# Performance work log

Measured on AMD Instinct MI355X. Metric: run time of the kernel, lower is better.

Reference implementation:

```python
import jax, jax.numpy as jnp
import numpy as np

N_MEL = 80
ENC_POS = 512 + 32  # encoder_output_dim + positional_embedding_dim
RNN = 1024
PRE = 256
B = 32
T = 800


def setup_inputs() -> dict:
    key = jax.random.key(0)
    ks = jax.random.split(key, 20)
    s = 0.05
    inp = {
        'duration_outputs': jax.random.normal(ks[0], (B, T, ENC_POS), jnp.float32),
        'decoder_inputs': jax.random.normal(ks[1], (B, N_MEL, T), jnp.float32),
        'memory_lengths': jax.random.randint(ks[2], (B,), 1, 200),
        # Prenet (no bias)
        'W1': jax.random.normal(ks[3], (PRE, N_MEL), jnp.float32) * s,
        'W2': jax.random.normal(ks[4], (PRE, PRE), jnp.float32) * s,
        # LSTMCellNorm 1: input = PRE + ENC_POS
        'Wih1': jax.random.normal(ks[5], (4 * RNN, PRE + ENC_POS), jnp.float32) * s,
        'Whh1': jax.random.normal(ks[6], (4 * RNN, RNN), jnp.float32) * s,
        'b1': jnp.zeros((4 * RNN,), jnp.float32),
        'g1': jnp.ones((4 * RNN,), jnp.float32),
        'be1': jnp.zeros((4 * RNN,), jnp.float32),
        # LSTMCellNorm 2
        'Wih2': jax.random.normal(ks[7], (4 * RNN, RNN), jnp.float32) * s,
        'Whh2': jax.random.normal(ks[8], (4 * RNN, RNN), jnp.float32) * s,
        'b2': jnp.zeros((4 * RNN,), jnp.float32),
        'g2': jnp.ones((4 * RNN,), jnp.float32),
        'be2': jnp.zeros((4 * RNN,), jnp.float32),
        # Linear projection: RNN + ENC_POS -> N_MEL
        'Wp': jax.random.normal(ks[9], (N_MEL, RNN + ENC_POS), jnp.float32) * s,
        'bp': jnp.zeros((N_MEL,), jnp.float32),
        # Dropout masks (prenet p=0.5 always on; decoder p=0.1 in training)
        'pm1': jax.random.bernoulli(ks[10], 0.5, (T + 1, B, PRE)).astype(jnp.float32) / 0.5,
        'pm2': jax.random.bernoulli(ks[11], 0.5, (T + 1, B, PRE)).astype(jnp.float32) / 0.5,
        'dm1': jax.random.bernoulli(ks[12], 0.9, (T, B, RNN)).astype(jnp.float32) / 0.9,
        'dm2': jax.random.bernoulli(ks[13], 0.9, (T, B, RNN)).astype(jnp.float32) / 0.9,
    }
    return inp


def _ln(z, g, b):
    m = jnp.mean(z, -1, keepdims=True)
    v = jnp.var(z, -1, keepdims=True)
    return (z - m) * jax.lax.rsqrt(v + 1e-5) * g + b


def _cell(x, h, c, Wih, Whh, bias, g, be):
    # layer-normalized LSTM cell: LN over the 4H pre-activation gates
    gates = _ln(x @ Wih.T + h @ Whh.T + bias, g, be)
    i, f, gg, o = jnp.split(gates, 4, axis=-1)
    c = jax.nn.sigmoid(f) * c + jax.nn.sigmoid(i) * jnp.tanh(gg)
    h = jax.nn.sigmoid(o) * jnp.tanh(c)
    return h, c


def reference(duration_outputs, decoder_inputs, memory_lengths,
              W1, W2, Wih1, Whh1, b1, g1, be1, Wih2, Whh2, b2, g2, be2,
              Wp, bp, pm1, pm2, dm1, dm2):
    Bv = duration_outputs.shape[0]
    H = Whh1.shape[1]
    # parse_decoder_inputs: [B, n_mel, T] -> [T, B, n_mel] (n_frames_per_step=1)
    dec = jnp.transpose(decoder_inputs, (2, 0, 1))
    Tv = dec.shape[0]
    go = jnp.zeros((1, Bv, dec.shape[2]), dec.dtype)
    dec = jnp.concatenate([go, dec], axis=0)  # [T+1, B, n_mel]
    # Prenet (dropout always active)
    x = jax.nn.relu(dec @ W1.T) * pm1
    x = jax.nn.relu(x @ W2.T) * pm2  # [T+1, B, PRE]
    dur = jnp.transpose(duration_outputs, (1, 0, 2))  # [T, B, 544]

    def step(carry, xs):
        h1, c1, h2, c2 = carry
        pre_t, dur_t, m1, m2 = xs
        h1, c1 = _cell(jnp.concatenate([pre_t, dur_t], -1), h1, c1, Wih1, Whh1, b1, g1, be1)
        h1 = h1 * m1  # dropped hidden is also carried, matching torch
        h2, c2 = _cell(h1, h2, c2, Wih2, Whh2, b2, g2, be2)
        h2 = h2 * m2
        out = jnp.concatenate([h2, dur_t], -1) @ Wp.T + bp
        return (h1, c1, h2, c2), out

    z = jnp.zeros((Bv, H), duration_outputs.dtype)
    _, outs = jax.lax.scan(step, (z, z, z, z), (x[:Tv], dur[:Tv], dm1, dm2))
    mel = jnp.transpose(outs, (1, 0, 2))  # [B, T, n_mel]
    mel = mel.reshape(Bv, -1, N_MEL)
    return jnp.transpose(mel, (0, 2, 1))  # [B, n_mel, T]
```

## Files before the change

### kernel.cpp

```cpp
#include <hip/hip_runtime.h>

#define TT 800
#define BB 32
#define HH 1024
#define G4 4096
#define PRE 256
#define DUR 544
#define XK 800
#define KA 1824
#define KB 2048
#define NM 80
#define KP 1568

#define SA 1864
#define SB 2056
#define SA1 104

#define OFF_WIH1B  0ull
#define OFF_WHH1B  6553600ull
#define OFF_WIH2B  14942208ull
#define OFF_WHH2B  23330816ull
#define OFF_WPB    31719424ull
#define OFF_W1B    31970304ull
#define OFF_W2B    32019456ull
#define OFF_XCAT   32150528ull
#define OFF_X1     73110528ull
#define OFF_H1H    86217728ull
#define OFF_H2H    138646528ull
#define OFF_PART1  191075328ull
#define OFF_PART2  191337472ull
#define OFF_FLAGS  191599616ull
#define FLAG_BYTES 217600ull
#define WS_NEEDED  (OFF_FLAGS + FLAG_BYTES)

#define LDS_SLAB_OFF  131584
#define LDS_STAT_OFF  148480
#define LDS_RED_OFF   148736
#define LDS_HPK_OFF   149760
#define LDS_TOTAL     150272

typedef __attribute__((ext_vector_type(8))) _Float16 f16x8;
typedef __attribute__((ext_vector_type(4))) float f32x4;
typedef unsigned long long ull;

__device__ __forceinline__ unsigned short f2h(float f) {
    _Float16 h = (_Float16)f;
    return __builtin_bit_cast(unsigned short, h);
}
__device__ __forceinline__ float sigf(float x) { return 1.f / (1.f + __expf(-x)); }
__device__ __forceinline__ float tanh_fast(float x) { return 1.f - 2.f / (__expf(2.f * x) + 1.f); }

__device__ __forceinline__ f16x8 ldg8(const unsigned short* p) {
    return *reinterpret_cast<const f16x8*>(p);
}

__device__ __forceinline__ f16x8 ld_h16(const ull* p) {
    union { ull u[2]; f16x8 v; } x;
    x.u[0] = __hip_atomic_load(p,     __ATOMIC_RELAXED, __HIP_MEMORY_SCOPE_AGENT);
    x.u[1] = __hip_atomic_load(p + 1, __ATOMIC_RELAXED, __HIP_MEMORY_SCOPE_AGENT);
    return x.v;
}
__device__ __forceinline__ float ld_cf(const float* p) {
    return __hip_atomic_load(p, __ATOMIC_RELAXED, __HIP_MEMORY_SCOPE_AGENT);
}
__device__ __forceinline__ void st_cf(float* p, float v) {
    __hip_atomic_store(p, v, __ATOMIC_RELAXED, __HIP_MEMORY_SCOPE_AGENT);
}

__device__ __forceinline__ void spin_until(int* p, int target) {
    while (__hip_atomic_load(p, __ATOMIC_RELAXED, __HIP_MEMORY_SCOPE_AGENT) < target)
        __builtin_amdgcn_s_sleep(1);
}

#define WAIT_VM0() __builtin_amdgcn_s_waitcnt(0x0F70)

__global__ void cvt_kernel(const float* __restrict__ src, unsigned short* __restrict__ dst, int n) {
    for (int i = blockIdx.x * blockDim.x + threadIdx.x; i < n; i += gridDim.x * blockDim.x)
        dst[i] = f2h(src[i]);
}

__global__ void cvt_w1_kernel(const float* __restrict__ w1, unsigned short* __restrict__ dst) {
    int i = blockIdx.x * blockDim.x + threadIdx.x;
    if (i >= 256 * 96) return;
    int j = i / 96, m = i % 96;
    dst[i] = (m < 80) ? f2h(w1[j * 80 + m]) : 0;
}

__global__ void pack_dur_kernel(const float* __restrict__ dur, unsigned short* __restrict__ xcat) {
    int n = TT * BB * DUR;
    for (int i = blockIdx.x * blockDim.x + threadIdx.x; i < n; i += gridDim.x * blockDim.x) {
        int t = i / (BB * DUR);
        int r = i % (BB * DUR);
        int b = r / DUR, e = r % DUR;
        xcat[(size_t)(t * BB + b) * XK + PRE + e] = f2h(dur[(size_t)b * (TT * DUR) + t * DUR + e]);
    }
}

__global__ __launch_bounds__(256) void prenet1_kernel(const float* __restrict__ din,
                                                      const unsigned short* __restrict__ w1b,
                                                      const float* __restrict__ pm1,
                                                      unsigned short* __restrict__ x1b) {
    int t = blockIdx.x;
    __shared__ unsigned short decs[32 * SA1];
    int tid = threadIdx.x;
    for (int idx = tid; idx < 32 * 96; idx += 256) {
        int b = idx / 96, m = idx % 96;
        float v = (m < 80 && t > 0) ? din[(size_t)b * 64000 + m * 800 + (t - 1)] : 0.f;
        decs[b * SA1 + m] = f2h(v);
    }
    __syncthreads();
    int lane = tid & 63, wid = tid >> 6;
    int l15 = lane & 15, quad = lane >> 4;
    int kblk = quad * 8;
    #pragma unroll
    for (int i = 0; i < 8; i++) {
        int tt = wid * 8 + i;
        int Mt = tt & 1, Nt = tt >> 1;
        f32x4 acc = {0.f, 0.f, 0.f, 0.f};
        int arow = (Mt * 16 + l15) * SA1 + kblk;
        int brow = (Nt * 16 + l15) * 96 + kblk;
        #pragma unroll
        for (int kk = 0; kk < 3; kk++) {
            f16x8 a = *reinterpret_cast<const f16x8*>(&decs[arow + kk * 32]);
            f16x8 b = ldg8(w1b + brow + kk * 32);
            acc = __builtin_amdgcn_mfma_f32_16x16x32_f16(a, b, acc, 0, 0, 0);
        }
        int n = Nt * 16 + l15;
        #pragma unroll
        for (int r = 0; r < 4; r++) {
            int b_row = Mt * 16 + quad * 4 + r;
            float v = fmaxf(acc[r], 0.f) * pm1[(size_t)(t * BB + b_row) * PRE + n];
            x1b[(size_t)(t * BB + b_row) * PRE + n] = f2h(v);
        }
    }
}

__global__ __launch_bounds__(256) void prenet2_kernel(const unsigned short* __restrict__ x1b,
                                                      const unsigned short* __restrict__ w2b,
                                                      const float* __restrict__ pm2,
                                                      unsigned short* __restrict__ xcat) {
    int t = blockIdx.x;
    int tid = threadIdx.x;
    int lane = tid & 63, wid = tid >> 6;
    int l15 = lane & 15, quad = lane >> 4;
    int kblk = quad * 8;
    #pragma unroll
    for (int i = 0; i < 8; i++) {
        int tt = wid * 8 + i;
        int Mt = tt & 1, Nt = tt >> 1;
        f32x4 acc = {0.f, 0.f, 0.f, 0.f};
        const unsigned short* arow = x1b + (size_t)(t * BB + Mt * 16 + l15) * PRE + kblk;
        const unsigned short* brow = w2b + (size_t)(Nt * 16 + l15) * PRE + kblk;
        #pragma unroll
        for (int kk = 0; kk < 8; kk++) {
            f16x8 a = ldg8(arow + kk * 32);
            f16x8 b = ldg8(brow + kk * 32);
            acc = __builtin_amdgcn_mfma_f32_16x16x32_f16(a, b, acc, 0, 0, 0);
        }
        int n = Nt * 16 + l15;
        #pragma unroll
        for (int r = 0; r < 4; r++) {
            int b_row = Mt * 16 + quad * 4 + r;
            float v = fmaxf(acc[r], 0.f) * pm2[(size_t)(t * BB + b_row) * PRE + n];
            xcat[(size_t)(t * BB + b_row) * XK + n] = f2h(v);
        }
    }
}

__global__ __launch_bounds__(256, 1) void persistent_kernel(
    const unsigned short* __restrict__ xcat,
    const unsigned short* __restrict__ wih1b, const unsigned short* __restrict__ whh1b,
    const unsigned short* __restrict__ wih2b, const unsigned short* __restrict__ whh2b,
    const float* __restrict__ b1, const float* __restrict__ g1, const float* __restrict__ be1,
    const float* __restrict__ b2, const float* __restrict__ g2, const float* __restrict__ be2,
    const float* __restrict__ dm1, const float* __restrict__ dm2,
    unsigned short* __restrict__ h1h, unsigned short* __restrict__ h2h,
    float* __restrict__ part1, float* __restrict__ part2,
    int* __restrict__ flags) {

    extern __shared__ char smem[];
    unsigned short* W = (unsigned short*)smem;
    float* slab = (float*)(smem + LDS_SLAB_OFF);
    float* stat = (float*)(smem + LDS_STAT_OFF);
    float* red  = (float*)(smem + LDS_RED_OFF);
    unsigned short* hpack = (unsigned short*)(smem + LDS_HPK_OFF);

    int wg = blockIdx.x;
    bool isA = wg < 128;
    int w = isA ? wg : wg - 128;
    int tid = threadIdx.x;
    int lane = tid & 63;
    int kid = tid >> 6;
    int l15 = lane & 15, quad = lane >> 4;
    int koff = quad * 8;

    int* r_h1     = flags + 800;
    int* gbase    = flags + 3200;
    int* r_stats  = isA ? flags : (flags + 1600);
    int* r_hmy    = isA ? (flags + 800) : (flags + 2400);
    int* g_stats  = isA ? gbase : (gbase + 25600);
    int* g_hmy    = isA ? (gbase + 12800) : (gbase + 38400);
    float* part   = isA ? part1 : part2;
    float* statg  = part + 4 * 8192;
    int gidx = w >> 3;
    bool isRed = (w == 0);

    if (isA) {
        for (int idx = tid; idx < 32 * KA; idx += 256) {
            int r = idx / KA, k = idx % KA;
            int grow = (r >> 3) * HH + w * 8 + (r & 7);
            W[r * SA + k] = (k < XK) ? wih1b[(size_t)grow * XK + k]
                                     : whh1b[(size_t)grow * HH + (k - XK)];
        }
    } else {
        for (int idx = tid; idx < 32 * KB; idx += 256) {
            int r = idx / KB, k = idx % KB;
            int grow = (r >> 3) * HH + w * 8 + (r & 7);
            W[r * SB + k] = (k < HH) ? wih2b[(size_t)grow * HH + k]
                                     : whh2b[(size_t)grow * HH + (k - HH)];
        }
    }

    int n_s = tid & 31, ms = (tid >> 5) * 4;
    int gate_ns = (n_s >> 3) * HH + w * 8 + (n_s & 7);
    float bsum = isA ? b1[gate_ns] : b2[gate_ns];

    int pb = tid & 31, pu = tid >> 5;
    int unit = w * 8 + pu;
    float g1v[4], bev[4];
    {
        const float* gs = isA ? g1 : g2;
        const float* bs = isA ? be1 : be2;
        #pragma unroll
        for (int g = 0; g < 4; g++) { g1v[g] = gs[g * HH + unit]; bev[g] = bs[g * HH + unit]; }
    }
    const float* dms = isA ? dm1 : dm2;
    unsigned short* hout = isA ? h1h : h2h;
    float* myslab = slab + kid * (32 * 33);
    int stride_slab = 33;
    float creg = 0.f;
    __syncthreads();

    for (int t = 0; t < TT; t++) {
        int slot = t & 3;
        f32x4 a00 = {0,0,0,0}, a01 = {0,0,0,0}, a10 = {0,0,0,0}, a11 = {0,0,0,0};

        if (isA) {
            const unsigned short* xb = xcat + (size_t)(t * BB) * XK;
            for (int kk = kid; kk < 25; kk += 4) {
                int k0 = kk * 32 + koff;
                f16x8 x0 = ldg8(xb + (size_t)(l15)      * XK + k0);
                f16x8 x1 = ldg8(xb + (size_t)(16 + l15) * XK + k0);
                f16x8 w0 = *(const f16x8*)&W[(l15)      * SA + k0];
                f16x8 w1 = *(const f16x8*)&W[(16 + l15) * SA + k0];
                a00 = __builtin_amdgcn_mfma_f32_16x16x32_f16(x0, w0, a00, 0, 0, 0);
                a01 = __builtin_amdgcn_mfma_f32_16x16x32_f16(x0, w1, a01, 0, 0, 0);
                a10 = __builtin_amdgcn_mfma_f32_16x16x32_f16(x1, w0, a10, 0, 0, 0);
                a11 = __builtin_amdgcn_mfma_f32_16x16x32_f16(x1, w1, a11, 0, 0, 0);
            }
            if (t > 0) {
                if (tid == 0) spin_until(&r_hmy[t - 1], 16);
                __syncthreads();
                const unsigned short* hb = h1h + (size_t)((t - 1) * BB) * HH;
                for (int kk = kid; kk < 32; kk += 4) {
                    int k0 = kk * 32 + koff;
                    f16x8 x0 = ld_h16((const ull*)(hb + (size_t)(l15)      * HH + k0));
                    f16x8 x1 = ld_h16((const ull*)(hb + (size_t)(16 + l15) * HH + k0));
                    f16x8 w0 = *(const f16x8*)&W[(l15)      * SA + XK + k0];
                    f16x8 w1 = *(const f16x8*)&W[(16 + l15) * SA + XK + k0];
                    a00 = __builtin_amdgcn_mfma_f32_16x16x32_f16(x0, w0, a00, 0, 0, 0);
                    a01 = __builtin_amdgcn_mfma_f32_16x16x32_f16(x0, w1, a01, 0, 0, 0);
                    a10 = __builtin_amdgcn_mfma_f32_16x16x32_f16(x1, w0, a10, 0, 0, 0);
                    a11 = __builtin_amdgcn_mfma_f32_16x16x32_f16(x1, w1, a11, 0, 0, 0);
                }
            }
        } else {
            if (t > 0) {
                if (tid == 0) spin_until(&r_hmy[t - 1], 16);
                __syncthreads();
                const unsigned short* hb = h2h + (size_t)((t - 1) * BB) * HH;
                for (int kk = kid; kk < 32; kk += 4) {
                    int k0 = kk * 32 + koff;
                    f16x8 x0 = ld_h16((const ull*)(hb + (size_t)(l15)      * HH + k0));
                    f16x8 x1 = ld_h16((const ull*)(hb + (size_t)(16 + l15) * HH + k0));
                    f16x8 w0 = *(const f16x8*)&W[(l15)      * SB + HH + k0];
                    f16x8 w1 = *(const f16x8*)&W[(16 + l15) * SB + HH + k0];
                    a00 = __builtin_amdgcn_mfma_f32_16x16x32_f16(x0, w0, a00, 0, 0, 0);
                    a01 = __builtin_amdgcn_mfma_f32_16x16x32_f16(x0, w1, a01, 0, 0, 0);
                    a10 = __builtin_amdgcn_mfma_f32_16x16x32_f16(x1, w0, a10, 0, 0, 0);
                    a11 = __builtin_amdgcn_mfma_f32_16x16x32_f16(x1, w1, a11, 0, 0, 0);
                }
            }
            if (tid == 0) spin_until(&r_h1[t], 16);
            __syncthreads();
            const unsigned short* hb = h1h + (size_t)(t * BB) * HH;
            for (int kk = kid; kk < 32; kk += 4) {
                int k0 = kk * 32 + koff;
                f16x8 x0 = ld_h16((const ull*)(hb + (size_t)(l15)      * HH + k0));
                f16x8 x1 = ld_h16((const ull*)(hb + (size_t)(16 + l15) * HH + k0));
                f16x8 w0 = *(const f16x8*)&W[(l15)      * SB + k0];
                f16x8 w1 = *(const f16x8*)&W[(16 + l15) * SB + k0];
                a00 = __builtin_amdgcn_mfma_f32_16x16x32_f16(x0, w0, a00, 0, 0, 0);
                a01 = __builtin_amdgcn_mfma_f32_16x16x32_f16(x0, w1, a01, 0, 0, 0);
                a10 = __builtin_amdgcn_mfma_f32_16x16x32_f16(x1, w0, a10, 0, 0, 0);
                a11 = __builtin_amdgcn_mfma_f32_16x16x32_f16(x1, w1, a11, 0, 0, 0);
            }
        }

        #pragma unroll
        for (int r = 0; r < 4; r++) {
            int m0 = quad * 4 + r;
            myslab[(l15)      * stride_slab + m0]      = a00[r];
            myslab[(16 + l15) * stride_slab + m0]      = a01[r];
            myslab[(l15)      * stride_slab + 16 + m0] = a10[r];
            myslab[(16 + l15) * stride_slab + 16 + m0] = a11[r];
        }
        __syncthreads();

        {
            int base = n_s * stride_slab + ms;
            #pragma unroll
            for (int j = 0; j < 4; j++) {
                float v = slab[base + j] + slab[1056 + base + j]
                        + slab[2112 + base + j] + slab[3168 + base + j] + bsum;
                slab[base + j] = v;
            }
        }
        __syncthreads();

        if (tid < 64) {
            int b = tid & 31, st = tid >> 5;
            float s = 0.f;
            #pragma unroll 8
            for (int n = 0; n < 32; n++) { float v = slab[n * stride_slab + b]; s += st ? v * v : v; }
            st_cf(&part[slot * 8192 + w * 64 + tid], s);
        }
        if (tid == 0) {
            WAIT_VM0();
            int old = __hip_atomic_fetch_add(&g_stats[t * 16 + gidx], 1,
                                             __ATOMIC_RELAXED, __HIP_MEMORY_SCOPE_AGENT);
            if (old == 7)
                __hip_atomic_fetch_add(&r_stats[t], 1,
                                       __ATOMIC_RELAXED, __HIP_MEMORY_SCOPE_AGENT);
        }

        if (isRed) {
            if (tid == 0) spin_until(&r_stats[t], 16);
            __syncthreads();
            {
                const float* pp = part + slot * 8192;
                float s = 0.f;
                int wp = tid >> 6, j = tid & 63;
                #pragma unroll
                for (int i = 0; i < 32; i++)
                    s += ld_cf(&pp[(wp + i * 4) * 64 + j]);
                red[tid] = s;
            }
            __syncthreads();
            if (tid < 64)
                st_cf(&statg[slot * 64 + tid],
                      red[tid] + red[64 + tid] + red[128 + tid] + red[192 + tid]);
            if (tid == 0) {
                WAIT_VM0();
                __hip_atomic_fetch_add(&r_stats[t], 1,
                                       __ATOMIC_RELAXED, __HIP_MEMORY_SCOPE_AGENT);
            }
        }

        if (tid == 0) spin_until(&r_stats[t], 17);
        __syncthreads();
        if (tid < 64) stat[tid] = ld_cf(&statg[slot * 64 + tid]);
        __syncthreads();

        {
            float mean = stat[pb] * (1.f / 4096.f);
            float var = stat[32 + pb] * (1.f / 4096.f) - mean * mean;
            float rs = rsqrtf(var + 1e-5f);
            float z[4];
            #pragma unroll
            for (int g = 0; g < 4; g++)
                z[g] = (slab[(g * 8 + pu) * stride_slab + pb] - mean) * rs * g1v[g] + bev[g];
            float iv = sigf(z[0]), fv = sigf(z[1]), gv = tanh_fast(z[2]), ov = sigf(z[3]);
            creg = fv * creg + iv * gv;
            float h = ov * tanh_fast(creg);
            h *= dms[(size_t)(t * BB + pb) * HH + unit];
            hpack[pb * 8 + pu] = f2h(h);
        }
        __syncthreads();

        if (tid < 64) {
            int b = tid >> 1, half = tid & 1;
            ull v = *(const ull*)((const char*)hpack + tid * 8);
            __hip_atomic_store((ull*)(hout + (size_t)(t * BB + b) * HH + w * 8 + half * 4),
                               v, __ATOMIC_RELAXED, __HIP_MEMORY_SCOPE_AGENT);
        }
        if (tid == 0) {
            WAIT_VM0();
            int old = __hip_atomic_fetch_add(&g_hmy[t * 16 + gidx], 1,
                                             __ATOMIC_RELAXED, __HIP_MEMORY_SCOPE_AGENT);
            if (old == 7)
                __hip_atomic_fetch_add(&r_hmy[t], 1,
                                       __ATOMIC_RELAXED, __HIP_MEMORY_SCOPE_AGENT);
        }
    }
}

__global__ __launch_bounds__(256) void projection_kernel(const unsigned short* __restrict__ h2h,
                                                         const unsigned short* __restrict__ xcat,
                                                         const unsigned short* __restrict__ wpb,
                                                         const float* __restrict__ bp,
                                                         float* __restrict__ out) {
    int t = blockIdx.x;
    int tid = threadIdx.x;
    int lane = tid & 63, wid = tid >> 6;
    int l15 = lane & 15, quad = lane >> 4;
    int kblk = quad * 8;
    #pragma unroll
    for (int i = 0; i < 3; i++) {
        int tt = wid + i * 4;
        if (tt >= 10) break;
        int Mt = tt & 1, Nt = tt >> 1;
        f32x4 acc = {0.f, 0.f, 0.f, 0.f};
        int b_row = Mt * 16 + l15;
        const unsigned short* h2row = h2h + (size_t)(t * BB + b_row) * HH + kblk;
        const unsigned short* brow = wpb + (size_t)(Nt * 16 + l15) * KP + kblk;
        #pragma unroll
        for (int kk = 0; kk < 32; kk++) {
            f16x8 a = ldg8(h2row + kk * 32);
            f16x8 b = ldg8(brow + kk * 32);
            acc = __builtin_amdgcn_mfma_f32_16x16x32_f16(a, b, acc, 0, 0, 0);
        }
        const unsigned short* drow = xcat + (size_t)(t * BB + b_row) * XK + PRE + kblk;
        #pragma unroll
        for (int kk = 0; kk < 17; kk++) {
            f16x8 a = ldg8(drow + kk * 32);
            f16x8 b = ldg8(brow + HH + kk * 32);
            acc = __builtin_amdgcn_mfma_f32_16x16x32_f16(a, b, acc, 0, 0, 0);
        }
        int mel = Nt * 16 + l15;
        float bpv = bp[mel];
        #pragma unroll
        for (int r = 0; r < 4; r++) {
            int b = Mt * 16 + quad * 4 + r;
            out[(size_t)b * 64000 + mel * 800 + t] = acc[r] + bpv;
        }
    }
}

extern "C" void kernel_launch(void* const* d_in, const int* in_sizes, int n_in,
                              void* d_out, int out_size, void* d_ws, size_t ws_size,
                              hipStream_t stream) {
    (void)in_sizes; (void)n_in; (void)out_size;
    const float* dur  = (const float*)d_in[0];
    const float* din  = (const float*)d_in[1];
    const float* W1   = (const float*)d_in[3];
    const float* W2   = (const float*)d_in[4];
    const float* Wih1 = (const float*)d_in[5];
    const float* Whh1 = (const float*)d_in[6];
    const float* b1   = (const float*)d_in[7];
    const float* g1   = (const float*)d_in[8];
    const float* be1  = (const float*)d_in[9];
    const float* Wih2 = (const float*)d_in[10];
    const float* Whh2 = (const float*)d_in[11];
    const float* b2   = (const float*)d_in[12];
    const float* g2   = (const float*)d_in[13];
    const float* be2  = (const float*)d_in[14];
    const float* Wp   = (const float*)d_in[15];
    const float* bp   = (const float*)d_in[16];
    const float* pm1  = (const float*)d_in[17];
    const float* pm2  = (const float*)d_in[18];
    const float* dm1  = (const float*)d_in[19];
    const float* dm2  = (const float*)d_in[20];
    float* out = (float*)d_out;
    char* ws = (char*)d_ws;
    if (ws_size < WS_NEEDED) return;

    unsigned short* wih1b = (unsigned short*)(ws + OFF_WIH1B);
    unsigned short* whh1b = (unsigned short*)(ws + OFF_WHH1B);
    unsigned short* wih2b = (unsigned short*)(ws + OFF_WIH2B);
    unsigned short* whh2b = (unsigned short*)(ws + OFF_WHH2B);
    unsigned short* wpb   = (unsigned short*)(ws + OFF_WPB);
    unsigned short* w1b   = (unsigned short*)(ws + OFF_W1B);
    unsigned short* w2b   = (unsigned short*)(ws + OFF_W2B);
    unsigned short* xcat  = (unsigned short*)(ws + OFF_XCAT);
    unsigned short* x1b   = (unsigned short*)(ws + OFF_X1);
    unsigned short* h1h   = (unsigned short*)(ws + OFF_H1H);
    unsigned short* h2h   = (unsigned short*)(ws + OFF_H2H);
    float* part1 = (float*)(ws + OFF_PART1);
    float* part2 = (float*)(ws + OFF_PART2);
    int* flags   = (int*)(ws + OFF_FLAGS);

    hipMemsetAsync(flags, 0, FLAG_BYTES, stream);

    int thr = 256;
    cvt_kernel<<<4096, thr, 0, stream>>>(Wih1, wih1b, G4 * XK);
    cvt_kernel<<<4096, thr, 0, stream>>>(Whh1, whh1b, G4 * HH);
    cvt_kernel<<<4096, thr, 0, stream>>>(Wih2, wih2b, G4 * HH);
    cvt_kernel<<<4096, thr, 0, stream>>>(Whh2, whh2b, G4 * HH);
    cvt_kernel<<<512,  thr, 0, stream>>>(Wp, wpb, NM * KP);
    cvt_w1_kernel<<<(256 * 96 + 255) / 256, thr, 0, stream>>>(W1, w1b);
    cvt_kernel<<<256,  thr, 0, stream>>>(W2, w2b, 256 * 256);

    prenet1_kernel<<<TT, thr, 0, stream>>>(din, w1b, pm1, x1b);
    prenet2_kernel<<<TT, thr, 0, stream>>>(x1b, w2b, pm2, xcat);
    pack_dur_kernel<<<8192, thr, 0, stream>>>(dur, xcat);

    hipFuncSetAttribute((const void*)persistent_kernel,
                        hipFuncAttributeMaxDynamicSharedMemorySize, LDS_TOTAL);
    persistent_kernel<<<256, thr, LDS_TOTAL, stream>>>(
        xcat, wih1b, whh1b, wih2b, whh2b,
        b1, g1, be1, b2, g2, be2, dm1, dm2,
        h1h, h2h, part1, part2, flags);

    projection_kernel<<<TT, thr, 0, stream>>>(h2h, xcat, wpb, bp, out);
}
```

Measured before the change: 15.56 ms.

## Replace two-level flag reduction with atomic stat accumulation and 16-flag polling

Removes the dedicated reducer workgroup that summed per-workgroup LayerNorm partials. Each workgroup now atomically adds its sums into a per-timestep accumulator, and waiters poll all 16 group counters directly instead of a second-level root flag. The input-projection MFMA for the next timestep is moved to run while waiting for the stats barrier, and the dropout mask load is hoisted to the top of the step. This shortens the critical path per timestep at the cost of float atomic contention and a larger memset, and atomic adds make the summation order nondeterministic.

```diff
diff --git a/kernel.cpp b/kernel.cpp
--- a/kernel.cpp
+++ b/kernel.cpp
@@ -35,9 +35,8 @@
 
 #define LDS_SLAB_OFF  131584
 #define LDS_STAT_OFF  148480
-#define LDS_RED_OFF   148736
-#define LDS_HPK_OFF   149760
-#define LDS_TOTAL     150272
+#define LDS_HPK_OFF   148736
+#define LDS_TOTAL     149248
 
 typedef __attribute__((ext_vector_type(8))) _Float16 f16x8;
 typedef __attribute__((ext_vector_type(4))) float f32x4;
@@ -63,13 +62,18 @@
 __device__ __forceinline__ float ld_cf(const float* p) {
     return __hip_atomic_load(p, __ATOMIC_RELAXED, __HIP_MEMORY_SCOPE_AGENT);
 }
-__device__ __forceinline__ void st_cf(float* p, float v) {
-    __hip_atomic_store(p, v, __ATOMIC_RELAXED, __HIP_MEMORY_SCOPE_AGENT);
-}
-
-__device__ __forceinline__ void spin_until(int* p, int target) {
-    while (__hip_atomic_load(p, __ATOMIC_RELAXED, __HIP_MEMORY_SCOPE_AGENT) < target)
-        __builtin_amdgcn_s_sleep(1);
+
+__device__ __forceinline__ void poll16(int* g, int target) {
+    for (;;) {
+        int m = 1 << 30;
+        #pragma unroll
+        for (int i = 0; i < 16; i++) {
+            int v = __hip_atomic_load(&g[i], __ATOMIC_RELAXED, __HIP_MEMORY_SCOPE_AGENT);
+            m = min(m, v);
+        }
+        if (m >= target) return;
+        __builtin_amdgcn_s_sleep(2);
+    }
 }
 
 #define WAIT_VM0() __builtin_amdgcn_s_waitcnt(0x0F70)
@@ -182,7 +186,6 @@
     unsigned short* W = (unsigned short*)smem;
     float* slab = (float*)(smem + LDS_SLAB_OFF);
     float* stat = (float*)(smem + LDS_STAT_OFF);
-    float* red  = (float*)(smem + LDS_RED_OFF);
     unsigned short* hpack = (unsigned short*)(smem + LDS_HPK_OFF);
 
     int wg = blockIdx.x;
@@ -194,16 +197,14 @@
     int l15 = lane & 15, quad = lane >> 4;
     int koff = quad * 8;
 
-    int* r_h1     = flags + 800;
-    int* gbase    = flags + 3200;
-    int* r_stats  = isA ? flags : (flags + 1600);
-    int* r_hmy    = isA ? (flags + 800) : (flags + 2400);
-    int* g_stats  = isA ? gbase : (gbase + 25600);
-    int* g_hmy    = isA ? (gbase + 12800) : (gbase + 38400);
-    float* part   = isA ? part1 : part2;
-    float* statg  = part + 4 * 8192;
+    int* g_stats1 = flags;
+    int* g_h1     = flags + 12800;
+    int* g_stats2 = flags + 25600;
+    int* g_h2     = flags + 38400;
+    int* g_smy    = isA ? g_stats1 : g_stats2;
+    int* g_hmy    = isA ? g_h1 : g_h2;
+    float* sacc   = isA ? part1 : part2;
     int gidx = w >> 3;
-    bool isRed = (w == 0);
 
     if (isA) {
         for (int idx = tid; idx < 32 * KA; idx += 256) {
@@ -237,29 +238,33 @@
     const float* dms = isA ? dm1 : dm2;
     unsigned short* hout = isA ? h1h : h2h;
     float* myslab = slab + kid * (32 * 33);
-    int stride_slab = 33;
+    const int SS = 33;
     float creg = 0.f;
+
+    f32x4 a00 = {0,0,0,0}, a01 = {0,0,0,0}, a10 = {0,0,0,0}, a11 = {0,0,0,0};
     __syncthreads();
 
+    if (isA) {
+        const unsigned short* xb = xcat;
+        for (int kk = kid; kk < 25; kk += 4) {
+            int k0 = kk * 32 + koff;
+            f16x8 x0 = ldg8(xb + (size_t)(l15)      * XK + k0);
+            f16x8 x1 = ldg8(xb + (size_t)(16 + l15) * XK + k0);
+            f16x8 w0 = *(const f16x8*)&W[(l15)      * SA + k0];
+            f16x8 w1 = *(const f16x8*)&W[(16 + l15) * SA + k0];
+            a00 = __builtin_amdgcn_mfma_f32_16x16x32_f16(x0, w0, a00, 0, 0, 0);
+            a01 = __builtin_amdgcn_mfma_f32_16x16x32_f16(x0, w1, a01, 0, 0, 0);
+            a10 = __builtin_amdgcn_mfma_f32_16x16x32_f16(x1, w0, a10, 0, 0, 0);
+            a11 = __builtin_amdgcn_mfma_f32_16x16x32_f16(x1, w1, a11, 0, 0, 0);
+        }
+    }
+
     for (int t = 0; t < TT; t++) {
-        int slot = t & 3;
-        f32x4 a00 = {0,0,0,0}, a01 = {0,0,0,0}, a10 = {0,0,0,0}, a11 = {0,0,0,0};
+        float dmv = dms[(size_t)(t * BB + pb) * HH + unit];
 
         if (isA) {
-            const unsigned short* xb = xcat + (size_t)(t * BB) * XK;
-            for (int kk = kid; kk < 25; kk += 4) {
-                int k0 = kk * 32 + koff;
-                f16x8 x0 = ldg8(xb + (size_t)(l15)      * XK + k0);
-                f16x8 x1 = ldg8(xb + (size_t)(16 + l15) * XK + k0);
-                f16x8 w0 = *(const f16x8*)&W[(l15)      * SA + k0];
-                f16x8 w1 = *(const f16x8*)&W[(16 + l15) * SA + k0];
-                a00 = __builtin_amdgcn_mfma_f32_16x16x32_f16(x0, w0, a00, 0, 0, 0);
-                a01 = __builtin_amdgcn_mfma_f32_16x16x32_f16(x0, w1, a01, 0, 0, 0);
-                a10 = __builtin_amdgcn_mfma_f32_16x16x32_f16(x1, w0, a10, 0, 0, 0);
-                a11 = __builtin_amdgcn_mfma_f32_16x16x32_f16(x1, w1, a11, 0, 0, 0);
-            }
             if (t > 0) {
-                if (tid == 0) spin_until(&r_hmy[t - 1], 16);
+                if (tid == 0) poll16(&g_h1[(t - 1) * 16], 8);
                 __syncthreads();
                 const unsigned short* hb = h1h + (size_t)((t - 1) * BB) * HH;
                 for (int kk = kid; kk < 32; kk += 4) {
@@ -275,8 +280,9 @@
                 }
             }
         } else {
+            a00 = a01 = a10 = a11 = (f32x4){0,0,0,0};
             if (t > 0) {
-                if (tid == 0) spin_until(&r_hmy[t - 1], 16);
+                if (tid == 0) poll16(&g_h2[(t - 1) * 16], 8);
                 __syncthreads();
                 const unsigned short* hb = h2h + (size_t)((t - 1) * BB) * HH;
                 for (int kk = kid; kk < 32; kk += 4) {
@@ -291,7 +297,7 @@
                     a11 = __builtin_amdgcn_mfma_f32_16x16x32_f16(x1, w1, a11, 0, 0, 0);
                 }
             }
-            if (tid == 0) spin_until(&r_h1[t], 16);
+            if (tid == 0) poll16(&g_h1[t * 16], 8);
             __syncthreads();
             const unsigned short* hb = h1h + (size_t)(t * BB) * HH;
             for (int kk = kid; kk < 32; kk += 4) {
@@ -310,15 +316,15 @@
         #pragma unroll
         for (int r = 0; r < 4; r++) {
             int m0 = quad * 4 + r;
-            myslab[(l15)      * stride_slab + m0]      = a00[r];
-            myslab[(16 + l15) * stride_slab + m0]      = a01[r];
-            myslab[(l15)      * stride_slab + 16 + m0] = a10[r];
-            myslab[(16 + l15) * stride_slab + 16 + m0] = a11[r];
+            myslab[(l15)      * SS + m0]      = a00[r];
+            myslab[(16 + l15) * SS + m0]      = a01[r];
+            myslab[(l15)      * SS + 16 + m0] = a10[r];
+            myslab[(16 + l15) * SS + 16 + m0] = a11[r];
         }
         __syncthreads();
 
         {
-            int base = n_s * stride_slab + ms;
+            int base = n_s * SS + ms;
             #pragma unroll
             for (int j = 0; j < 4; j++) {
                 float v = slab[base + j] + slab[1056 + base + j]
@@ -332,44 +338,35 @@
             int b = tid & 31, st = tid >> 5;
             float s = 0.f;
             #pragma unroll 8
-            for (int n = 0; n < 32; n++) { float v = slab[n * stride_slab + b]; s += st ? v * v : v; }
-            st_cf(&part[slot * 8192 + w * 64 + tid], s);
+            for (int n = 0; n < 32; n++) { float v = slab[n * SS + b]; s += st ? v * v : v; }
+            __hip_atomic_fetch_add(&sacc[t * 64 + tid], s,
+                                   __ATOMIC_RELAXED, __HIP_MEMORY_SCOPE_AGENT);
         }
         if (tid == 0) {
             WAIT_VM0();
-            int old = __hip_atomic_fetch_add(&g_stats[t * 16 + gidx], 1,
-                                             __ATOMIC_RELAXED, __HIP_MEMORY_SCOPE_AGENT);
-            if (old == 7)
-                __hip_atomic_fetch_add(&r_stats[t], 1,
-                                       __ATOMIC_RELAXED, __HIP_MEMORY_SCOPE_AGENT);
-        }
-
-        if (isRed) {
-            if (tid == 0) spin_until(&r_stats[t], 16);
-            __syncthreads();
-            {
-                const float* pp = part + slot * 8192;
-                float s = 0.f;
-                int wp = tid >> 6, j = tid & 63;
-                #pragma unroll
-                for (int i = 0; i < 32; i++)
-                    s += ld_cf(&pp[(wp + i * 4) * 64 + j]);
-                red[tid] = s;
+            __hip_atomic_fetch_add(&g_smy[t * 16 + gidx], 1,
+                                   __ATOMIC_RELAXED, __HIP_MEMORY_SCOPE_AGENT);
+        }
+
+        if (isA && t + 1 < TT) {
+            a00 = a01 = a10 = a11 = (f32x4){0,0,0,0};
+            const unsigned short* xb = xcat + (size_t)((t + 1) * BB) * XK;
+            for (int kk = kid; kk < 25; kk += 4) {
+                int k0 = kk * 32 + koff;
+                f16x8 x0 = ldg8(xb + (size_t)(l15)      * XK + k0);
+                f16x8 x1 = ldg8(xb + (size_t)(16 + l15) * XK + k0);
+                f16x8 w0 = *(const f16x8*)&W[(l15)      * SA + k0];
+                f16x8 w1 = *(const f16x8*)&W[(16 + l15) * SA + k0];
+                a00 = __builtin_amdgcn_mfma_f32_16x16x32_f16(x0, w0, a00, 0, 0, 0);
+                a01 = __builtin_amdgcn_mfma_f32_16x16x32_f16(x0, w1, a01, 0, 0, 0);
+                a10 = __builtin_amdgcn_mfma_f32_16x16x32_f16(x1, w0, a10, 0, 0, 0);
+                a11 = __builtin_amdgcn_mfma_f32_16x16x32_f16(x1, w1, a11, 0, 0, 0);
             }
-            __syncthreads();
-            if (tid < 64)
-                st_cf(&statg[slot * 64 + tid],
-                      red[tid] + red[64 + tid] + red[128 + tid] + red[192 + tid]);
-            if (tid == 0) {
-                WAIT_VM0();
-                __hip_atomic_fetch_add(&r_stats[t], 1,
-                                       __ATOMIC_RELAXED, __HIP_MEMORY_SCOPE_AGENT);
-            }
-        }
-
-        if (tid == 0) spin_until(&r_stats[t], 17);
+        }
+
+        if (tid == 0) poll16(&g_smy[t * 16], 8);
         __syncthreads();
-        if (tid < 64) stat[tid] = ld_cf(&statg[slot * 64 + tid]);
+        if (tid < 64) stat[tid] = ld_cf(&sacc[t * 64 + tid]);
         __syncthreads();
 
         {
@@ -379,11 +376,11 @@
             float z[4];
             #pragma unroll
             for (int g = 0; g < 4; g++)
-                z[g] = (slab[(g * 8 + pu) * stride_slab + pb] - mean) * rs * g1v[g] + bev[g];
+                z[g] = (slab[(g * 8 + pu) * SS + pb] - mean) * rs * g1v[g] + bev[g];
             float iv = sigf(z[0]), fv = sigf(z[1]), gv = tanh_fast(z[2]), ov = sigf(z[3]);
             creg = fv * creg + iv * gv;
             float h = ov * tanh_fast(creg);
-            h *= dms[(size_t)(t * BB + pb) * HH + unit];
+            h *= dmv;
             hpack[pb * 8 + pu] = f2h(h);
         }
         __syncthreads();
@@ -396,11 +393,8 @@
         }
         if (tid == 0) {
             WAIT_VM0();
-            int old = __hip_atomic_fetch_add(&g_hmy[t * 16 + gidx], 1,
-                                             __ATOMIC_RELAXED, __HIP_MEMORY_SCOPE_AGENT);
-            if (old == 7)
-                __hip_atomic_fetch_add(&r_hmy[t], 1,
-                                       __ATOMIC_RELAXED, __HIP_MEMORY_SCOPE_AGENT);
+            __hip_atomic_fetch_add(&g_hmy[t * 16 + gidx], 1,
+                                   __ATOMIC_RELAXED, __HIP_MEMORY_SCOPE_AGENT);
         }
     }
 }
@@ -490,7 +484,7 @@
     float* part2 = (float*)(ws + OFF_PART2);
     int* flags   = (int*)(ws + OFF_FLAGS);
 
-    hipMemsetAsync(flags, 0, FLAG_BYTES, stream);
+    hipMemsetAsync(ws + OFF_PART1, 0, (OFF_FLAGS - OFF_PART1) + FLAG_BYTES, stream);
 
     int thr = 256;
     cvt_kernel<<<4096, thr, 0, stream>>>(Wih1, wih1b, G4 * XK);
```

Measured after the change: 16.75 ms. 7.6% more time.
